# Kernel tuning notes

Measured on AMD Instinct MI355X. Metric: run time of the kernel, lower is better.

Reference implementation:

```python
import jax, jax.numpy as jnp
import numpy as np

N = 50000       # nodes
E = 800000      # edges
IN = 64         # input node feature dim
H = 4           # attention heads
C = 32          # per-head channels (h_dim)
HC = H * C      # 128, concat output per conv
ED = 16         # edge feature dim
G = 2000        # number of graphs (molecules)
NEG = 0.2       # GATConv negative slope


def setup_inputs() -> dict:
    key = jax.random.key(0)
    ks = jax.random.split(key, 40)
    rn = lambda k, shp, s=0.1: (jax.random.normal(k, shp, jnp.float32) * s)
    inp = {}
    inp["x"] = jax.random.normal(ks[0], (N, IN), jnp.float32)
    inp["edge_index"] = jax.random.randint(ks[1], (2, E), 0, N)
    inp["edge_attr"] = jax.random.normal(ks[2], (E, ED), jnp.float32)
    inp["batch"] = jnp.sort(jax.random.randint(ks[3], (N,), 0, G))
    dins = [IN, HC, HC]
    i = 4
    for l in (1, 2, 3):
        din = dins[l - 1]
        inp[f"W{l}"] = rn(ks[i], (din, HC)); i += 1
        inp[f"as{l}"] = rn(ks[i], (H, C)); i += 1
        inp[f"ad{l}"] = rn(ks[i], (H, C)); i += 1
        inp[f"We{l}"] = rn(ks[i], (ED, HC)); i += 1
        inp[f"ae{l}"] = rn(ks[i], (H, C)); i += 1
        inp[f"b{l}"] = rn(ks[i], (HC,)); i += 1
    D = 4 * HC
    inp["lw1"] = rn(ks[i], (D, D)); i += 1
    inp["lb1"] = rn(ks[i], (D,)); i += 1
    inp["lw2"] = rn(ks[i], (D, 1)); i += 1
    inp["lb2"] = rn(ks[i], (1,)); i += 1
    return inp


def gat_conv(x, src, dst, edge_attr, W, a_s, a_d, We, a_e, b):
    n = x.shape[0]
    h = (x @ W).reshape(n, H, C)                       # [N,H,C]
    alpha_src = (h * a_s).sum(-1)                      # [N,H]
    alpha_dst = (h * a_d).sum(-1)                      # [N,H]
    he = (edge_attr @ We).reshape(-1, H, C)            # [E,H,C]
    alpha_edge = (he * a_e).sum(-1)                    # [E,H]
    alpha = jax.nn.leaky_relu(alpha_src[src] + alpha_dst[dst] + alpha_edge, NEG)
    # per-destination softmax over incoming edges (stable)
    amax = jax.ops.segment_max(alpha, dst, num_segments=n)
    amax = jnp.where(jnp.isfinite(amax), amax, 0.0)
    ex = jnp.exp(alpha - amax[dst])                    # [E,H]
    denom = jax.ops.segment_sum(ex, dst, num_segments=n)
    w = ex / (denom[dst] + 1e-16)                      # [E,H]
    m = h[src] * w[:, :, None]                         # [E,H,C]
    out = jax.ops.segment_sum(m, dst, num_segments=n)  # [N,H,C]
    return out.reshape(n, HC) + b


def reference(x, edge_index, edge_attr, batch,
              W1, as1, ad1, We1, ae1, b1,
              W2, as2, ad2, We2, ae2, b2,
              W3, as3, ad3, We3, ae3, b3,
              lw1, lb1, lw2, lb2):
    src, dst = edge_index[0], edge_index[1]
    h1 = gat_conv(x, src, dst, edge_attr, W1, as1, ad1, We1, ae1, b1)
    h2 = gat_conv(h1, src, dst, edge_attr, W2, as2, ad2, We2, ae2, b2)
    h3 = gat_conv(h2, src, dst, edge_attr, W3, as3, ad3, We3, ae3, b3)
    h_pool = jax.ops.segment_sum(h3, batch, num_segments=G)  # global_add_pool
    h_pool_ = h_pool[batch]                                  # == repeat_interleave by counts
    h = jnp.concatenate([h1, h2, h3, h_pool_], axis=1)       # [N, 4*HC]
    h = jax.nn.leaky_relu(h @ lw1 + lb1, 0.01)               # torch LeakyReLU default
    return h @ lw2 + lb2                                     # [N, 1]
```

## Files before the change

kernel.cpp:

```cpp
#include <hip/hip_runtime.h>
#include <hip/hip_bf16.h>
#include <math.h>

#define NN 50000
#define NNP 50048
#define NE 800000
#define DIN1 64
#define NHEAD 4
#define CH 32
#define HC 128
#define EDIM 16
#define NG 2000
#define MAXCH 64

typedef __attribute__((ext_vector_type(8))) short short8;
typedef __attribute__((ext_vector_type(4))) float floatx4;

__device__ __forceinline__ float lrelu(float x, float s) { return x > 0.f ? x : s * x; }

__device__ __forceinline__ unsigned short f2bf(float x) {
  unsigned int u = __float_as_uint(x);
  u += 0x7fff + ((u >> 16) & 1);
  return (unsigned short)(u >> 16);
}
__device__ __forceinline__ float bflo(unsigned int u) { return __uint_as_float(u << 16); }
__device__ __forceinline__ float bfhi(unsigned int u) { return __uint_as_float(u & 0xffff0000u); }

__device__ __forceinline__ void async16(void* lds, const void* g) {
  __builtin_amdgcn_global_load_lds((const __attribute__((address_space(1))) unsigned int*)g,
                                   (__attribute__((address_space(3))) unsigned int*)lds, 16, 0, 0);
}

#define NB_WEA 1
#define NB_WSD 24
#define NB_LW1T 768
#define NB_WT 160
#define NB_CAST 12500
#define NB_GST 196
#define NB_OUT 196
#define NB_HIST 3125
#define PREP_BLOCKS (NB_WEA + NB_WSD + NB_LW1T + NB_WT + NB_CAST + NB_GST + NB_OUT + NB_HIST)

__global__ __launch_bounds__(256) void k_prep(
    const float* __restrict__ We1, const float* __restrict__ ae1,
    const float* __restrict__ We2, const float* __restrict__ ae2,
    const float* __restrict__ We3, const float* __restrict__ ae3, float* __restrict__ wea,
    const float* __restrict__ W1, const float* __restrict__ as1, const float* __restrict__ ad1,
    const float* __restrict__ W2, const float* __restrict__ as2, const float* __restrict__ ad2,
    const float* __restrict__ W3, const float* __restrict__ as3, const float* __restrict__ ad3,
    unsigned short* __restrict__ wsdb,
    const float* __restrict__ lw1, unsigned short* __restrict__ lw1img,
    unsigned short* __restrict__ wtb,
    const float* __restrict__ x, unsigned short* __restrict__ xb0,
    const int* __restrict__ batch, int* __restrict__ gs,
    float* __restrict__ out, const float* __restrict__ lb2,
    const int* __restrict__ dstp, int* __restrict__ cnt) {
  int b = blockIdx.x;
  int t = threadIdx.x;
  if (b < NB_WEA) {
    if (t >= 3 * EDIM * NHEAD) return;
    int l = t / (EDIM * NHEAD);
    int rem = t % (EDIM * NHEAD);
    int d = rem / NHEAD, h = rem % NHEAD;
    const float* We = (l == 0) ? We1 : ((l == 1) ? We2 : We3);
    const float* ae = (l == 0) ? ae1 : ((l == 1) ? ae2 : ae3);
    float s = 0.f;
    for (int c = 0; c < CH; ++c) s += We[d * HC + h * CH + c] * ae[h * CH + c];
    wea[t] = s;
    return;
  }
  b -= NB_WEA;
  if (b < NB_WSD) {
    int i = b * 256 + t;
    int l = i >> 11;
    int col = (i >> 7) & 15;
    int k = i & 127;
    size_t oidx = (size_t)l * 2048 + ((size_t)(k >> 3) * 16 + col) * 8 + (k & 7);
    if (col >= 8 || (l == 0 && k >= DIN1)) { wsdb[oidx] = 0; return; }
    const float* W = (l == 0) ? W1 : ((l == 1) ? W2 : W3);
    int head = col & 3;
    const float* av = (col < 4) ? ((l == 0) ? as1 : ((l == 1) ? as2 : as3))
                                : ((l == 0) ? ad1 : ((l == 1) ? ad2 : ad3));
    float s = 0.f;
    for (int c = 0; c < CH; ++c) s += W[(size_t)k * HC + head * CH + c] * av[head * CH + c];
    wsdb[oidx] = f2bf(s);
    return;
  }
  b -= NB_WSD;
  if (b < NB_LW1T) {
    int i = b * 256 + t;
    int j = i / 384, k = i % 384;
    int jh = j >> 8, jc = j & 255;
    lw1img[((size_t)jh * 48 * 256 + (size_t)(k >> 3) * 256 + jc) * 8 + (k & 7)] =
        f2bf(lw1[(size_t)k * 512 + j]);
    return;
  }
  b -= NB_LW1T;
  if (b < NB_WT) {
    int i = b * 256 + t;
    const float* W;
    int j, k;
    size_t base;
    if (i < 128 * 64) {
      W = W1; j = i / 64; k = i % 64; base = 0;
    } else if (i < 128 * 64 + 128 * 128) {
      int ii = i - 128 * 64;
      W = W2; j = ii / 128; k = ii % 128; base = 8192;
    } else {
      int ii = i - (128 * 64 + 128 * 128);
      W = W3; j = ii / 128; k = ii % 128; base = 24576;
    }
    wtb[base + ((size_t)(k >> 3) * 128 + j) * 8 + (k & 7)] = f2bf(W[(size_t)k * HC + j]);
    return;
  }
  b -= NB_WT;
  if (b < NB_CAST) {
    int i = b * 256 + t;
    int n = i >> 6, k = i & 63;
    xb0[((size_t)(k >> 3) * NNP + n) * 8 + (k & 7)] = f2bf(x[i]);
    return;
  }
  b -= NB_CAST;
  if (b < NB_GST) {
    int i = b * 256 + t;
    if (i >= NN) return;
    int bb = batch[i];
    if (i == 0) {
      for (int g = 0; g <= bb; ++g) gs[g] = 0;
    } else {
      int pb = batch[i - 1];
      for (int g = pb + 1; g <= bb; ++g) gs[g] = i;
    }
    if (i == NN - 1) {
      for (int g = bb + 1; g <= NG; ++g) gs[g] = NN;
    }
    return;
  }
  b -= NB_GST;
  if (b < NB_OUT) {
    int i = b * 256 + t;
    if (i < NN) out[i] = lb2[0];
    return;
  }
  b -= NB_OUT;
  {
    int e = b * 256 + t;
    if (e < NE) atomicAdd(&cnt[dstp[e]], 1);
  }
}

__global__ __launch_bounds__(256) void k_scan1(const int* __restrict__ cnt, int* __restrict__ row_start,
                                               int* __restrict__ aux) {
  __shared__ int s[256];
  int t = threadIdx.x;
  int i = blockIdx.x * 256 + t;
  int v = (i < NN) ? cnt[i] : 0;
  s[t] = v;
  __syncthreads();
  for (int off = 1; off < 256; off <<= 1) {
    int tv = (t >= off) ? s[t - off] : 0;
    __syncthreads();
    s[t] += tv;
    __syncthreads();
  }
  if (i < NN) row_start[i] = s[t] - v;
  if (t == 255) aux[blockIdx.x] = s[255];
}

__global__ __launch_bounds__(256) void k_scan2(int* __restrict__ aux, int nb) {
  __shared__ int s[256];
  int t = threadIdx.x;
  int v = (t < nb) ? aux[t] : 0;
  s[t] = v;
  __syncthreads();
  for (int off = 1; off < 256; off <<= 1) {
    int tv = (t >= off) ? s[t - off] : 0;
    __syncthreads();
    s[t] += tv;
    __syncthreads();
  }
  if (t < nb) aux[t] = s[t] - v;
}

__global__ __launch_bounds__(256) void k_scan3(int* __restrict__ row_start, const int* __restrict__ aux) {
  int i = blockIdx.x * 256 + threadIdx.x;
  if (i < NN) row_start[i] += aux[i >> 8];
  else if (i == NN) row_start[NN] = NE;
}

__global__ __launch_bounds__(256) void k_scatter(const int* __restrict__ dst, const int* __restrict__ row_start,
                                                 int* __restrict__ fill, int* __restrict__ perm) {
  int e = blockIdx.x * 256 + threadIdx.x;
  if (e >= NE) return;
  int d = dst[e];
  int p = atomicAdd(&fill[d], 1);
  perm[row_start[d] + p] = e;
}

__global__ __launch_bounds__(256) void k_permute(const int* __restrict__ perm, const int* __restrict__ src,
                                                 const float* __restrict__ edge_attr, const float* __restrict__ wea,
                                                 int* __restrict__ srcp, float* __restrict__ aep) {
  __shared__ float wl[3 * EDIM * NHEAD];
  int t = threadIdx.x;
  if (t < 3 * EDIM * NHEAD) wl[t] = wea[t];
  __syncthreads();
  int pos = blockIdx.x * 256 + t;
  if (pos >= NE) return;
  int e = perm[pos];
  srcp[pos] = src[e];
  float ea[EDIM];
#pragma unroll
  for (int k = 0; k < EDIM; k += 4) {
    float4 v = *(const float4*)&edge_attr[(size_t)e * EDIM + k];
    ea[k] = v.x; ea[k + 1] = v.y; ea[k + 2] = v.z; ea[k + 3] = v.w;
  }
#pragma unroll
  for (int l = 0; l < 3; ++l) {
    float a0 = 0.f, a1 = 0.f, a2 = 0.f, a3 = 0.f;
#pragma unroll
    for (int k = 0; k < EDIM; ++k) {
      float ev = ea[k];
      a0 += ev * wl[l * 64 + k * 4 + 0];
      a1 += ev * wl[l * 64 + k * 4 + 1];
      a2 += ev * wl[l * 64 + k * 4 + 2];
      a3 += ev * wl[l * 64 + k * 4 + 3];
    }
    *(float4*)&aep[(size_t)l * NE * 4 + (size_t)pos * 4] = make_float4(a0, a1, a2, a3);
  }
}

template <int K>
__global__ __launch_bounds__(256) void k_conv_mfma(const unsigned short* __restrict__ xin,
                                                   const unsigned short* __restrict__ wt,
                                                   const unsigned short* __restrict__ wsd,
                                                   unsigned short* __restrict__ htb,
                                                   float* __restrict__ asrc, float* __restrict__ adst) {
  constexpr int NC = K / 8;
  constexpr int CA = NC * 128;
  constexpr int CB2 = NC * 16;
  __shared__ unsigned short As[CA * 8];
  __shared__ unsigned short Bs[CA * 8];
  __shared__ unsigned short Bs2[CB2 * 8];
  int t = threadIdx.x;
  int n0 = blockIdx.x * 128;
  int lane = t & 63;
  int wave = t >> 6;
  int wr = wave >> 1, wc = wave & 1;

  floatx4 acc[4][4];
  floatx4 acce[4];
#pragma unroll
  for (int a = 0; a < 4; ++a) {
    acce[a] = (floatx4){0.f, 0.f, 0.f, 0.f};
#pragma unroll
    for (int b = 0; b < 4; ++b) acc[a][b] = (floatx4){0.f, 0.f, 0.f, 0.f};
  }

  for (int c0 = wave * 64; c0 < CA; c0 += 256) {
    int kc = c0 >> 7, row0 = c0 & 127;
    async16(As + (size_t)c0 * 8, xin + ((size_t)kc * NNP + n0 + row0 + lane) * 8);
    async16(Bs + (size_t)c0 * 8, wt + ((size_t)c0 + lane) * 8);
  }
  if (wave * 64 < CB2) async16(Bs2 + (size_t)wave * 64 * 8, wsd + ((size_t)wave * 64 + lane) * 8);

  __syncthreads();

  int frow = lane & 15, fkc = lane >> 4;
#pragma unroll
  for (int kk = 0; kk < K / 32; ++kk) {
    const unsigned short* ab = As + (size_t)(kk * 4 + fkc) * 128 * 8;
    const unsigned short* bb = Bs + (size_t)(kk * 4 + fkc) * 128 * 8;
    short8 af[4], bf[4], bf2;
#pragma unroll
    for (int ti = 0; ti < 4; ++ti) af[ti] = *(const short8*)(ab + ((size_t)(wr * 64 + frow + ti * 16)) * 8);
#pragma unroll
    for (int tj = 0; tj < 4; ++tj) bf[tj] = *(const short8*)(bb + ((size_t)(wc * 64 + frow + tj * 16)) * 8);
    bf2 = *(const short8*)(Bs2 + ((size_t)(kk * 4 + fkc) * 16 + frow) * 8);
#pragma unroll
    for (int ti = 0; ti < 4; ++ti)
#pragma unroll
      for (int tj = 0; tj < 4; ++tj)
        acc[ti][tj] = __builtin_amdgcn_mfma_f32_16x16x32_bf16(af[ti], bf[tj], acc[ti][tj], 0, 0, 0);
    if (wc == 0) {
#pragma unroll
      for (int ti = 0; ti < 4; ++ti)
        acce[ti] = __builtin_amdgcn_mfma_f32_16x16x32_bf16(af[ti], bf2, acce[ti], 0, 0, 0);
    }
  }

  int q = lane & 15;
  int colg = wc * 64 + q;
#pragma unroll
  for (int ti = 0; ti < 4; ++ti) {
    int rowb = n0 + wr * 64 + ti * 16 + (lane >> 4) * 4;
#pragma unroll
    for (int r = 0; r < 4; ++r) {
      int row = rowb + r;
      if (row < NN) {
        htb[(size_t)row * HC + colg] = f2bf(acc[ti][0][r]);
        htb[(size_t)row * HC + colg + 16] = f2bf(acc[ti][1][r]);
        htb[(size_t)row * HC + colg + 32] = f2bf(acc[ti][2][r]);
        htb[(size_t)row * HC + colg + 48] = f2bf(acc[ti][3][r]);
        if (wc == 0 && q < 8) {
          float v = acce[ti][r];
          if (q < 4) asrc[row * 4 + q] = v;
          else adst[row * 4 + (q - 4)] = v;
        }
      }
    }
  }
}

__global__ __launch_bounds__(256) void k_aggregate(
    const unsigned short* __restrict__ htb, const int* __restrict__ srcp,
    const float* __restrict__ aep, const float* __restrict__ asrc, const float* __restrict__ adst,
    const int* __restrict__ row_start, const float* __restrict__ bias,
    unsigned short* __restrict__ XBp, int kcoff) {
  __shared__ float exs[4][MAXCH][4];
  int t = threadIdx.x;
  int lane = t & 63, wid = t >> 6;
  int n = blockIdx.x * 4 + wid;
  if (n >= NN) return;
  int rs = row_start[n], re = row_start[n + 1];
  int nchunk = (re - rs + MAXCH - 1) / MAXCH;
  int q = lane & 15, g = lane >> 4;
  int h = q >> 2;
  float4 ad4 = *(const float4*)&adst[n * 4];
  float acc[8];
#pragma unroll
  for (int j = 0; j < 8; ++j) acc[j] = 0.f;
  float d0 = 0.f, d1 = 0.f, d2 = 0.f, d3 = 0.f;

  for (int cc = 0; cc < nchunk; ++cc) {
    int base = rs + cc * MAXCH;
    int m = re - base;
    if (m > MAXCH) m = MAXCH;
    if (lane < m) {
      int i = base + lane;
      int s = srcp[i];
      float4 ae = *(const float4*)&aep[(size_t)i * 4];
      float4 as4 = *(const float4*)&asrc[s * 4];
      float4 ex;
      ex.x = __expf(lrelu(as4.x + ad4.x + ae.x, 0.2f));
      ex.y = __expf(lrelu(as4.y + ad4.y + ae.y, 0.2f));
      ex.z = __expf(lrelu(as4.z + ad4.z + ae.z, 0.2f));
      ex.w = __expf(lrelu(as4.w + ad4.w + ae.w, 0.2f));
      *(float4*)&exs[wid][lane][0] = ex;
      d0 += ex.x; d1 += ex.y; d2 += ex.z; d3 += ex.w;
    }
    __threadfence_block();
    int iters = (m + 7) >> 3;
    for (int kk = 0; kk < iters; ++kk) {
      int ii0 = kk * 8 + g;
      int ii1 = ii0 + 4;
      int i0 = base + ((ii0 < m) ? ii0 : 0);
      int i1 = base + ((ii1 < m) ? ii1 : 0);
      int s0 = srcp[i0];
      int s1 = srcp[i1];
      uint4 h0 = *(const uint4*)(htb + (size_t)s0 * HC + q * 8);
      uint4 h1 = *(const uint4*)(htb + (size_t)s1 * HC + q * 8);
      float w0 = (ii0 < m) ? exs[wid][ii0][h] : 0.f;
      float w1 = (ii1 < m) ? exs[wid][ii1][h] : 0.f;
      acc[0] += w0 * bflo(h0.x) + w1 * bflo(h1.x);
      acc[1] += w0 * bfhi(h0.x) + w1 * bfhi(h1.x);
      acc[2] += w0 * bflo(h0.y) + w1 * bflo(h1.y);
      acc[3] += w0 * bfhi(h0.y) + w1 * bfhi(h1.y);
      acc[4] += w0 * bflo(h0.z) + w1 * bflo(h1.z);
      acc[5] += w0 * bfhi(h0.z) + w1 * bfhi(h1.z);
      acc[6] += w0 * bflo(h0.w) + w1 * bflo(h1.w);
      acc[7] += w0 * bfhi(h0.w) + w1 * bfhi(h1.w);
    }
    __threadfence_block();
  }

#pragma unroll
  for (int mm = 1; mm < 64; mm <<= 1) {
    d0 += __shfl_xor(d0, mm, 64);
    d1 += __shfl_xor(d1, mm, 64);
    d2 += __shfl_xor(d2, mm, 64);
    d3 += __shfl_xor(d3, mm, 64);
  }
#pragma unroll
  for (int j = 0; j < 8; ++j) {
    acc[j] += __shfl_xor(acc[j], 16, 64);
    acc[j] += __shfl_xor(acc[j], 32, 64);
  }
  if (g == 0) {
    float dh = (h == 0) ? d0 : ((h == 1) ? d1 : ((h == 2) ? d2 : d3));
    float inv = 1.f / (dh + 1e-16f);
    unsigned int w[4];
#pragma unroll
    for (int j = 0; j < 4; ++j) {
      float v0 = acc[2 * j] * inv + bias[q * 8 + 2 * j];
      float v1 = acc[2 * j + 1] * inv + bias[q * 8 + 2 * j + 1];
      w[j] = (unsigned int)f2bf(v0) | ((unsigned int)f2bf(v1) << 16);
    }
    *(uint4*)&XBp[((size_t)(kcoff + q) * NNP + n) * 8] = make_uint4(w[0], w[1], w[2], w[3]);
  }
}

__global__ __launch_bounds__(128) void k_pool(const unsigned short* __restrict__ XBp, const int* __restrict__ gs,
                                              float* __restrict__ hpool) {
  int g = blockIdx.x;
  int j = threadIdx.x;
  int kc = 32 + (j >> 3), sb = j & 7;
  int s = gs[g], e = gs[g + 1];
  float acc = 0.f;
  for (int i = s; i < e; ++i) acc += bflo((unsigned int)XBp[((size_t)kc * NNP + i) * 8 + sb]);
  hpool[(size_t)g * HC + j] = acc;
}

__global__ __launch_bounds__(256) void k_pool_gemm(const float* __restrict__ hpool, const float* __restrict__ lw1,
                                                   float* __restrict__ ph) {
  __shared__ float hp[16][128];
  int t = threadIdx.x;
  int j0 = blockIdx.x * 128;
  int g0 = blockIdx.y * 16;
  int jj = t & 127, gg = t >> 7;
#pragma unroll
  for (int i = 0; i < 8; ++i) {
    int q = t + 256 * i;
    int row = q >> 7, col = q & 127;
    hp[row][col] = hpool[(size_t)(g0 + row) * HC + col];
  }
  __syncthreads();
  float acc[8];
#pragma unroll
  for (int i = 0; i < 8; ++i) acc[i] = 0.f;
  for (int k = 0; k < HC; ++k) {
    float wv = lw1[(size_t)(384 + k) * 512 + j0 + jj];
#pragma unroll
    for (int gi = 0; gi < 8; ++gi) acc[gi] += hp[gg + 2 * gi][k] * wv;
  }
#pragma unroll
  for (int gi = 0; gi < 8; ++gi) ph[(size_t)(g0 + gg + 2 * gi) * 512 + j0 + jj] = acc[gi];
}

__global__ __launch_bounds__(256, 2) void k_mlp_mfma(
    const unsigned short* __restrict__ XBp, const unsigned short* __restrict__ lw1img,
    const float* __restrict__ ph, const int* __restrict__ batch,
    const float* __restrict__ lb1, const float* __restrict__ lw2,
    float* __restrict__ out) {
  int t = threadIdx.x;
  int jh = blockIdx.x;
  int n0 = blockIdx.y * 128;
  int lane = t & 63;
  int wave = t >> 6;
  int wr = wave >> 1, wc = wave & 1;
  const unsigned short* bimg = lw1img + (size_t)jh * 48 * 256 * 8;

  floatx4 acc[4][8];
#pragma unroll
  for (int a = 0; a < 4; ++a)
#pragma unroll
    for (int b = 0; b < 8; ++b) acc[a][b] = (floatx4){0.f, 0.f, 0.f, 0.f};

  const unsigned short* abase = XBp + (((size_t)(lane >> 4)) * NNP + n0 + wr * 64 + (lane & 15)) * 8;
  const unsigned short* bbase = bimg + (((size_t)(lane >> 4)) * 256 + wc * 128 + (lane & 15)) * 8;
  const size_t akk = (size_t)4 * NNP * 8;
  const size_t bkk = (size_t)4 * 256 * 8;

  short8 af0[4], af1[4], bfE[8], bfO[8];
#pragma unroll
  for (int ti = 0; ti < 4; ++ti) af0[ti] = *(const short8*)(abase + (size_t)ti * 16 * 8);

#pragma unroll
  for (int kk2 = 0; kk2 < 6; ++kk2) {
    const unsigned short* ae_ = abase + (size_t)(2 * kk2) * akk;
    const unsigned short* be_ = bbase + (size_t)(2 * kk2) * bkk;
#pragma unroll
    for (int tj = 0; tj < 8; ++tj) bfE[tj] = *(const short8*)(be_ + (size_t)tj * 16 * 8);
#pragma unroll
    for (int ti = 0; ti < 4; ++ti) af1[ti] = *(const short8*)(ae_ + akk + (size_t)ti * 16 * 8);
#pragma unroll
    for (int ti = 0; ti < 4; ++ti)
#pragma unroll
      for (int tj = 0; tj < 8; ++tj)
        acc[ti][tj] = __builtin_amdgcn_mfma_f32_16x16x32_bf16(af0[ti], bfE[tj], acc[ti][tj], 0, 0, 0);
#pragma unroll
    for (int tj = 0; tj < 8; ++tj) bfO[tj] = *(const short8*)(be_ + bkk + (size_t)tj * 16 * 8);
    if (kk2 < 5) {
#pragma unroll
      for (int ti = 0; ti < 4; ++ti) af0[ti] = *(const short8*)(ae_ + 2 * akk + (size_t)ti * 16 * 8);
    }
#pragma unroll
    for (int ti = 0; ti < 4; ++ti)
#pragma unroll
      for (int tj = 0; tj < 8; ++tj)
        acc[ti][tj] = __builtin_amdgcn_mfma_f32_16x16x32_bf16(af1[ti], bfO[tj], acc[ti][tj], 0, 0, 0);
  }

  int colg = jh * 256 + wc * 128 + (lane & 15);
#pragma unroll
  for (int ti = 0; ti < 4; ++ti) {
    int rowb = n0 + wr * 64 + ti * 16 + (lane >> 4) * 4;
#pragma unroll
    for (int r = 0; r < 4; ++r) {
      int row = rowb + r;
      int rc = (row < NN) ? row : 0;
      int bg = batch[rc];
      float partial = 0.f;
#pragma unroll
      for (int tj = 0; tj < 8; ++tj) {
        int j = colg + tj * 16;
        float v = acc[ti][tj][r] + ph[(size_t)bg * 512 + j] + lb1[j];
        partial += lrelu(v, 0.01f) * lw2[j];
      }
#pragma unroll
      for (int m = 1; m < 16; m <<= 1) partial += __shfl_xor(partial, m, 16);
      if ((lane & 15) == 0 && row < NN) atomicAdd(&out[row], partial);
    }
  }
}

extern "C" void kernel_launch(void* const* d_in, const int* in_sizes, int n_in,
                              void* d_out, int out_size, void* d_ws, size_t ws_size,
                              hipStream_t stream) {
  const float* x = (const float*)d_in[0];
  const int* edge_index = (const int*)d_in[1];
  const int* src = edge_index;
  const int* dstp = edge_index + NE;
  const float* edge_attr = (const float*)d_in[2];
  const int* batch = (const int*)d_in[3];
  const float* W[3] = {(const float*)d_in[4], (const float*)d_in[10], (const float*)d_in[16]};
  const float* as_[3] = {(const float*)d_in[5], (const float*)d_in[11], (const float*)d_in[17]};
  const float* ad_[3] = {(const float*)d_in[6], (const float*)d_in[12], (const float*)d_in[18]};
  const float* We_[3] = {(const float*)d_in[7], (const float*)d_in[13], (const float*)d_in[19]};
  const float* ae_[3] = {(const float*)d_in[8], (const float*)d_in[14], (const float*)d_in[20]};
  const float* b_[3] = {(const float*)d_in[9], (const float*)d_in[15], (const float*)d_in[21]};
  const float* lw1 = (const float*)d_in[22];
  const float* lb1 = (const float*)d_in[23];
  const float* lw2 = (const float*)d_in[24];
  const float* lb2 = (const float*)d_in[25];
  float* out = (float*)d_out;

  float* f = (float*)d_ws;
  size_t o = 0;
  float* asrc = f + o;  o += (size_t)NN * NHEAD;
  float* adst = f + o;  o += (size_t)NN * NHEAD;
  float* wea = f + o;   o += 256;
  float* hpool = f + o; o += (size_t)NG * HC;
  float* aep = f + o;   o += (size_t)3 * NE * 4;
  unsigned short* xb0 = (unsigned short*)(f + o);
  float* ph = (float*)xb0;
  o += (size_t)8 * NNP * 8 / 2;
  unsigned short* htb = (unsigned short*)(f + o);   o += (size_t)NN * HC / 2;
  unsigned short* XB = (unsigned short*)(f + o);    o += (size_t)48 * NNP * 8 / 2;
  unsigned short* wtb = (unsigned short*)(f + o);   o += (size_t)(128 * 64 + 2 * 128 * 128) / 2;
  unsigned short* lw1img = (unsigned short*)(f + o); o += (size_t)2 * 48 * 256 * 8 / 2;
  unsigned short* wsdb = (unsigned short*)(f + o);  o += (size_t)3 * 2048 / 2;
  int* row_start = (int*)(f + o);
  int* cnt = row_start + (NN + 1);
  int* fill = cnt + NN;
  int* aux = fill + NN;
  int* gs = aux + 256;
  int* perm = gs + (NG + 1);
  int* srcp = perm + NE;

  const int NB = (NN + 255) / 256;
  const int EB = (NE + 255) / 256;

  hipMemsetAsync(cnt, 0, (size_t)2 * NN * sizeof(int), stream);

  k_prep<<<PREP_BLOCKS, 256, 0, stream>>>(
      We_[0], ae_[0], We_[1], ae_[1], We_[2], ae_[2], wea,
      W[0], as_[0], ad_[0], W[1], as_[1], ad_[1], W[2], as_[2], ad_[2], wsdb,
      lw1, lw1img, wtb, x, xb0, batch, gs, out, lb2, dstp, cnt);
  k_scan1<<<NB, 256, 0, stream>>>(cnt, row_start, aux);
  k_scan2<<<1, 256, 0, stream>>>(aux, NB);
  k_scan3<<<NB, 256, 0, stream>>>(row_start, aux);
  k_scatter<<<EB, 256, 0, stream>>>(dstp, row_start, fill, perm);
  k_permute<<<EB, 256, 0, stream>>>(perm, src, edge_attr, wea, srcp, aep);

  const int CONVB = NNP / 128;
  unsigned short* wt_l[3] = {wtb, wtb + 8192, wtb + 24576};
  for (int l = 0; l < 3; ++l) {
    unsigned short* wsd_l = wsdb + (size_t)l * 2048;
    const unsigned short* xin = (l == 0) ? xb0 : (XB + (size_t)(l - 1) * 16 * NNP * 8);
    if (l == 0)
      k_conv_mfma<64><<<CONVB, 256, 0, stream>>>(xin, wt_l[0], wsd_l, htb, asrc, adst);
    else
      k_conv_mfma<128><<<CONVB, 256, 0, stream>>>(xin, wt_l[l], wsd_l, htb, asrc, adst);
    k_aggregate<<<(NN + 3) / 4, 256, 0, stream>>>(htb, srcp, aep + (size_t)l * NE * 4, asrc, adst,
                                                  row_start, b_[l], XB, l * 16);
  }

  k_pool<<<NG, 128, 0, stream>>>(XB, gs, hpool);
  k_pool_gemm<<<dim3(4, NG / 16), 256, 0, stream>>>(hpool, lw1, ph);
  k_mlp_mfma<<<dim3(2, NNP / 128), 256, 0, stream>>>(XB, lw1img, ph, batch, lb1, lw2, out);
}
```

Before: 491.0 us.

## Shuffle source indices in aggregation, unroll 4 edges, reorder MLP GEMM pipeline and grid

```diff
diff --git a/kernel.cpp b/kernel.cpp
--- a/kernel.cpp
+++ b/kernel.cpp
@@ -335,11 +335,12 @@
     int base = rs + cc * MAXCH;
     int m = re - base;
     if (m > MAXCH) m = MAXCH;
+    int sreg = 0;
     if (lane < m) {
       int i = base + lane;
-      int s = srcp[i];
+      sreg = srcp[i];
       float4 ae = *(const float4*)&aep[(size_t)i * 4];
-      float4 as4 = *(const float4*)&asrc[s * 4];
+      float4 as4 = *(const float4*)&asrc[sreg * 4];
       float4 ex;
       ex.x = __expf(lrelu(as4.x + ad4.x + ae.x, 0.2f));
       ex.y = __expf(lrelu(as4.y + ad4.y + ae.y, 0.2f));
@@ -349,26 +350,30 @@
       d0 += ex.x; d1 += ex.y; d2 += ex.z; d3 += ex.w;
     }
     __threadfence_block();
-    int iters = (m + 7) >> 3;
-    for (int kk = 0; kk < iters; ++kk) {
-      int ii0 = kk * 8 + g;
-      int ii1 = ii0 + 4;
-      int i0 = base + ((ii0 < m) ? ii0 : 0);
-      int i1 = base + ((ii1 < m) ? ii1 : 0);
-      int s0 = srcp[i0];
-      int s1 = srcp[i1];
+    int rounds = (m + 15) >> 4;
+    for (int rr = 0; rr < rounds; ++rr) {
+      int ii0 = rr * 16 + g;
+      int ii1 = ii0 + 4, ii2 = ii0 + 8, ii3 = ii0 + 12;
+      int s0 = __shfl(sreg, ii0, 64);
+      int s1 = __shfl(sreg, ii1, 64);
+      int s2 = __shfl(sreg, ii2, 64);
+      int s3 = __shfl(sreg, ii3, 64);
       uint4 h0 = *(const uint4*)(htb + (size_t)s0 * HC + q * 8);
       uint4 h1 = *(const uint4*)(htb + (size_t)s1 * HC + q * 8);
+      uint4 h2 = *(const uint4*)(htb + (size_t)s2 * HC + q * 8);
+      uint4 h3 = *(const uint4*)(htb + (size_t)s3 * HC + q * 8);
       float w0 = (ii0 < m) ? exs[wid][ii0][h] : 0.f;
       float w1 = (ii1 < m) ? exs[wid][ii1][h] : 0.f;
-      acc[0] += w0 * bflo(h0.x) + w1 * bflo(h1.x);
-      acc[1] += w0 * bfhi(h0.x) + w1 * bfhi(h1.x);
-      acc[2] += w0 * bflo(h0.y) + w1 * bflo(h1.y);
-      acc[3] += w0 * bfhi(h0.y) + w1 * bfhi(h1.y);
-      acc[4] += w0 * bflo(h0.z) + w1 * bflo(h1.z);
-      acc[5] += w0 * bfhi(h0.z) + w1 * bfhi(h1.z);
-      acc[6] += w0 * bflo(h0.w) + w1 * bflo(h1.w);
-      acc[7] += w0 * bfhi(h0.w) + w1 * bfhi(h1.w);
+      float w2 = (ii2 < m) ? exs[wid][ii2][h] : 0.f;
+      float w3 = (ii3 < m) ? exs[wid][ii3][h] : 0.f;
+      acc[0] += w0 * bflo(h0.x) + w1 * bflo(h1.x) + w2 * bflo(h2.x) + w3 * bflo(h3.x);
+      acc[1] += w0 * bfhi(h0.x) + w1 * bfhi(h1.x) + w2 * bfhi(h2.x) + w3 * bfhi(h3.x);
+      acc[2] += w0 * bflo(h0.y) + w1 * bflo(h1.y) + w2 * bflo(h2.y) + w3 * bflo(h3.y);
+      acc[3] += w0 * bfhi(h0.y) + w1 * bfhi(h1.y) + w2 * bfhi(h2.y) + w3 * bfhi(h3.y);
+      acc[4] += w0 * bflo(h0.z) + w1 * bflo(h1.z) + w2 * bflo(h2.z) + w3 * bflo(h3.z);
+      acc[5] += w0 * bfhi(h0.z) + w1 * bfhi(h1.z) + w2 * bfhi(h2.z) + w3 * bfhi(h3.z);
+      acc[6] += w0 * bflo(h0.w) + w1 * bflo(h1.w) + w2 * bflo(h2.w) + w3 * bflo(h3.w);
+      acc[7] += w0 * bfhi(h0.w) + w1 * bfhi(h1.w) + w2 * bfhi(h2.w) + w3 * bfhi(h3.w);
     }
     __threadfence_block();
   }
@@ -441,9 +446,14 @@
     const float* __restrict__ ph, const int* __restrict__ batch,
     const float* __restrict__ lb1, const float* __restrict__ lw2,
     float* __restrict__ out) {
-  int t = threadIdx.x;
-  int jh = blockIdx.x;
-  int n0 = blockIdx.y * 128;
+  int bid = blockIdx.x;
+  int group = bid >> 4;
+  int idx = bid & 15;
+  int jh = idx >> 3;
+  int n0i = group * 8 + (idx & 7);
+  if (n0i >= NNP / 128) return;
+  int n0 = n0i * 128;
+  int t = threadIdx.x;
   int lane = t & 63;
   int wave = t >> 6;
   int wr = wave >> 1, wc = wave & 1;
@@ -460,34 +470,32 @@
   const size_t akk = (size_t)4 * NNP * 8;
   const size_t bkk = (size_t)4 * 256 * 8;
 
-  short8 af0[4], af1[4], bfE[8], bfO[8];
-#pragma unroll
-  for (int ti = 0; ti < 4; ++ti) af0[ti] = *(const short8*)(abase + (size_t)ti * 16 * 8);
-
-#pragma unroll
-  for (int kk2 = 0; kk2 < 6; ++kk2) {
-    const unsigned short* ae_ = abase + (size_t)(2 * kk2) * akk;
-    const unsigned short* be_ = bbase + (size_t)(2 * kk2) * bkk;
-#pragma unroll
-    for (int tj = 0; tj < 8; ++tj) bfE[tj] = *(const short8*)(be_ + (size_t)tj * 16 * 8);
-#pragma unroll
-    for (int ti = 0; ti < 4; ++ti) af1[ti] = *(const short8*)(ae_ + akk + (size_t)ti * 16 * 8);
+  short8 af[2][4], bf[2][8];
+#pragma unroll
+  for (int ti = 0; ti < 4; ++ti) af[0][ti] = *(const short8*)(abase + (size_t)ti * 16 * 8);
+#pragma unroll
+  for (int ti = 0; ti < 4; ++ti) af[1][ti] = *(const short8*)(abase + akk + (size_t)ti * 16 * 8);
+#pragma unroll
+  for (int tj = 0; tj < 8; ++tj) bf[0][tj] = *(const short8*)(bbase + (size_t)tj * 16 * 8);
+
+#pragma unroll
+  for (int kk = 0; kk < 12; ++kk) {
+    const int cur = kk & 1, nxt = cur ^ 1;
+    if (kk < 11) {
+      const unsigned short* bn = bbase + (size_t)(kk + 1) * bkk;
+#pragma unroll
+      for (int tj = 0; tj < 8; ++tj) bf[nxt][tj] = *(const short8*)(bn + (size_t)tj * 16 * 8);
+    }
 #pragma unroll
     for (int ti = 0; ti < 4; ++ti)
 #pragma unroll
       for (int tj = 0; tj < 8; ++tj)
-        acc[ti][tj] = __builtin_amdgcn_mfma_f32_16x16x32_bf16(af0[ti], bfE[tj], acc[ti][tj], 0, 0, 0);
-#pragma unroll
-    for (int tj = 0; tj < 8; ++tj) bfO[tj] = *(const short8*)(be_ + bkk + (size_t)tj * 16 * 8);
-    if (kk2 < 5) {
-#pragma unroll
-      for (int ti = 0; ti < 4; ++ti) af0[ti] = *(const short8*)(ae_ + 2 * akk + (size_t)ti * 16 * 8);
-    }
-#pragma unroll
-    for (int ti = 0; ti < 4; ++ti)
-#pragma unroll
-      for (int tj = 0; tj < 8; ++tj)
-        acc[ti][tj] = __builtin_amdgcn_mfma_f32_16x16x32_bf16(af1[ti], bfO[tj], acc[ti][tj], 0, 0, 0);
+        acc[ti][tj] = __builtin_amdgcn_mfma_f32_16x16x32_bf16(af[cur][ti], bf[cur][tj], acc[ti][tj], 0, 0, 0);
+    if (kk < 10) {
+      const unsigned short* an = abase + (size_t)(kk + 2) * akk;
+#pragma unroll
+      for (int ti = 0; ti < 4; ++ti) af[cur][ti] = *(const short8*)(an + (size_t)ti * 16 * 8);
+    }
   }
 
   int colg = jh * 256 + wc * 128 + (lane & 15);
@@ -587,5 +595,5 @@
 
   k_pool<<<NG, 128, 0, stream>>>(XB, gs, hpool);
   k_pool_gemm<<<dim3(4, NG / 16), 256, 0, stream>>>(hpool, lw1, ph);
-  k_mlp_mfma<<<dim3(2, NNP / 128), 256, 0, stream>>>(XB, lw1img, ph, batch, lb1, lw2, out);
-}
+  k_mlp_mfma<<<784, 256, 0, stream>>>(XB, lw1img, ph, batch, lb1, lw2, out);
+}
```

Result: no change. 496.4 us (+1.1%).
